# Kernel tuning notes

Hardware: AMD Instinct MI355X
Metric: run time of the kernel (lower is better)

The kernel has to match this reference:

```python
import jax, jax.numpy as jnp
import numpy as np

N_NODES = 50000
N_EDGES = 800000
IN_F, EDGE_F, HID, HEADS, OUT_F = 128, 16, 32, 4, 128
NEG_SLOPE = 0.2


def edge_gat_layer(h, ef, src, dst, W, We, al, ar, ae, b, act):
    """One DGL-style EdgeGATConv layer.
    h: [N, Fin], ef: [E, Fe], W: [Fin, H*D], We: [Fe, H*D],
    al/ar/ae: [H, D], b: [H*D]. Returns [N, H*D].
    """
    N = h.shape[0]
    H, D = al.shape
    feat = (h @ W).reshape(N, H, D)                    # [N,H,D]
    fe = (ef @ We).reshape(-1, H, D)                   # [E,H,D]
    el = jnp.einsum('nhd,hd->nh', feat, al)            # [N,H]
    er = jnp.einsum('nhd,hd->nh', feat, ar)            # [N,H]
    ee = jnp.einsum('ehd,hd->eh', fe, ae)              # [E,H]
    e = jax.nn.leaky_relu(el[src] + er[dst] + ee, NEG_SLOPE)  # [E,H]
    # edge softmax over incoming edges of each dst node
    emax = jax.ops.segment_max(e, dst, num_segments=N)        # [N,H]
    ex = jnp.exp(e - emax[dst])                               # [E,H]
    esum = jax.ops.segment_sum(ex, dst, num_segments=N)       # [N,H]
    a = ex / esum[dst]                                        # [E,H]
    msg = feat[src] * a[:, :, None]                           # [E,H,D]
    rst = jax.ops.segment_sum(msg, dst, num_segments=N)       # [N,H,D]
    rst = rst + b.reshape(1, H, D)
    if act:
        rst = jax.nn.relu(rst)
    return rst.reshape(N, H * D)


def _glorot(k, shape):
    fan = shape[0]
    return jax.random.normal(k, shape, dtype=jnp.float32) / np.sqrt(fan)


def setup_inputs() -> dict:
    key = jax.random.key(0)
    ks = jax.random.split(key, 24)
    inp = {
        'h': jax.random.normal(ks[0], (N_NODES, IN_F), dtype=jnp.float32),
        'edge_feats': jax.random.normal(ks[1], (N_EDGES, EDGE_F), dtype=jnp.float32),
        'src': jax.random.randint(ks[2], (N_EDGES,), 0, N_NODES, dtype=jnp.int32),
        'dst': jax.random.randint(ks[3], (N_EDGES,), 0, N_NODES, dtype=jnp.int32),
    }
    # layer 0: IN_F -> HEADS*HID ; layer 1: HEADS*HID -> HEADS*HID ; layer 2: heads=1, OUT_F
    dims = [(IN_F, HEADS, HID), (HEADS * HID, HEADS, HID), (HEADS * HID, 1, OUT_F)]
    ki = 4
    for i, (fin, H, D) in enumerate(dims):
        inp[f'W{i}'] = _glorot(ks[ki], (fin, H * D)); ki += 1
        inp[f'We{i}'] = _glorot(ks[ki], (EDGE_F, H * D)); ki += 1
        inp[f'al{i}'] = _glorot(ks[ki], (H, D)); ki += 1
        inp[f'ar{i}'] = _glorot(ks[ki], (H, D)); ki += 1
        inp[f'ae{i}'] = _glorot(ks[ki], (H, D)); ki += 1
        inp[f'b{i}'] = jnp.zeros((H * D,), dtype=jnp.float32)
    return inp


def reference(h, edge_feats, src, dst,
              W0, We0, al0, ar0, ae0, b0,
              W1, We1, al1, ar1, ae1, b1,
              W2, We2, al2, ar2, ae2, b2):
    h = edge_gat_layer(h, edge_feats, src, dst, W0, We0, al0, ar0, ae0, b0, True)
    h = edge_gat_layer(h, edge_feats, src, dst, W1, We1, al1, ar1, ae1, b1, True)
    h = edge_gat_layer(h, edge_feats, src, dst, W2, We2, al2, ar2, ae2, b2, False)
    return h
```

## Files before the change

kernel.cpp:

```cpp
#include <hip/hip_runtime.h>
#include <hip/hip_fp16.h>
#include <cstdint>

#define NN 50000
#define NE 800000
static constexpr int HD = 128;
static constexpr int EF_DIM = 16;
static constexpr int SCAN_B = 256;
static constexpr int NPARTS = (NN + SCAN_B - 1) / SCAN_B;

typedef _Float16 f16x4 __attribute__((ext_vector_type(4)));
typedef float f32x4 __attribute__((ext_vector_type(4)));

__global__ __launch_bounds__(256) void k_prep(const float* __restrict__ h,
        const float* __restrict__ We0, const float* __restrict__ ae0,
        const float* __restrict__ We1, const float* __restrict__ ae1,
        const float* __restrict__ We2, const float* __restrict__ ae2,
        const float* __restrict__ W0, const float* __restrict__ W1,
        const float* __restrict__ W2,
        int* __restrict__ deg, float* __restrict__ M,
        _Float16* __restrict__ Wht, _Float16* __restrict__ Xh) {
    const int b = blockIdx.x, t = threadIdx.x;
    if (b < 196) {
        int i = b * 256 + t;
        if (i < NN) deg[i] = 0;
        return;
    }
    if (b < 199) {
        int l = b - 196;
        const float* We = (l == 0) ? We0 : (l == 1) ? We1 : We2;
        const float* ae = (l == 0) ? ae0 : (l == 1) ? ae1 : ae2;
        int H = (l == 2) ? 1 : 4, D = (l == 2) ? 128 : 32;
        if (t < EF_DIM * H) {
            int f = t / H, hh = t % H;
            float s = 0.f;
            for (int d = 0; d < D; d++) s += We[f * HD + hh * D + d] * ae[hh * D + d];
            M[l * 64 + f * H + hh] = s;
        }
        return;
    }
    if (b < 391) {
        int i = (b - 199) * 256 + t;
        int l = i >> 14, rem = i & 16383;
        int n = rem >> 7, k = rem & 127;
        const float* W = (l == 0) ? W0 : (l == 1) ? W1 : W2;
        Wht[(size_t)l * 16384 + n * 128 + k] = (_Float16)W[k * 128 + n];
        return;
    }
    {
        int i = (b - 391) * 256 + t;
        if (i < NN * 32) {
            float4 v = ((const float4*)h)[i];
            f16x4 o = {(_Float16)v.x, (_Float16)v.y, (_Float16)v.z, (_Float16)v.w};
            ((f16x4*)Xh)[i] = o;
        }
    }
}


__global__ void k_hist(const int* __restrict__ dst, int* __restrict__ deg) {
    int e = blockIdx.x * blockDim.x + threadIdx.x;
    if (e < NE) atomicAdd(&deg[dst[e]], 1);
}

__global__ __launch_bounds__(SCAN_B) void k_part(const int* __restrict__ deg,
                                                 int* __restrict__ part) {
    __shared__ int s[SCAN_B];
    int t = threadIdx.x;
    int i = blockIdx.x * SCAN_B + t;
    s[t] = (i < NN) ? deg[i] : 0;
    __syncthreads();
    for (int off = SCAN_B / 2; off > 0; off >>= 1) {
        if (t < off) s[t] += s[t + off];
        __syncthreads();
    }
    if (t == 0) part[blockIdx.x] = s[0];
}

__global__ __launch_bounds__(SCAN_B) void k_scanpart(int* __restrict__ part) {
    __shared__ int s[SCAN_B];
    int t = threadIdx.x;
    int v = (t < NPARTS) ? part[t] : 0;
    s[t] = v;
    __syncthreads();
    for (int off = 1; off < SCAN_B; off <<= 1) {
        int u = (t >= off) ? s[t - off] : 0;
        __syncthreads();
        s[t] += u;
        __syncthreads();
    }
    if (t < NPARTS) part[t] = s[t] - v;
}

__global__ __launch_bounds__(SCAN_B) void k_rowptr(const int* __restrict__ deg,
                                                   const int* __restrict__ part,
                                                   int* __restrict__ row_ptr,
                                                   int* __restrict__ cursor) {
    __shared__ int s[SCAN_B];
    int t = threadIdx.x;
    int i = blockIdx.x * SCAN_B + t;
    int v = (i < NN) ? deg[i] : 0;
    s[t] = v;
    __syncthreads();
    for (int off = 1; off < SCAN_B; off <<= 1) {
        int u = (t >= off) ? s[t - off] : 0;
        __syncthreads();
        s[t] += u;
        __syncthreads();
    }
    int excl = s[t] - v + part[blockIdx.x];
    if (i < NN) { row_ptr[i] = excl; cursor[i] = excl; }
    if (i == NN) row_ptr[NN] = NE;
}

__global__ void k_scatter(const int* __restrict__ src, const int* __restrict__ dst,
                          int* __restrict__ cursor, int2* __restrict__ epr) {
    int e = blockIdx.x * blockDim.x + threadIdx.x;
    if (e >= NE) return;
    int d = dst[e];
    int pos = atomicAdd(&cursor[d], 1);
    epr[pos] = make_int2(e, src[e]);
}

__global__ __launch_bounds__(256) void k_segsort(const int* __restrict__ row_ptr,
                                                 int2* __restrict__ epr) {
    __shared__ int2 seg[4][128];
    const int wave = threadIdx.x >> 6;
    const int lane = threadIdx.x & 63;
    const int n = blockIdx.x * 4 + wave;
    const int start = row_ptr[n];
    const int len = row_ptr[n + 1] - start;
    const bool small = (len > 0 && len <= 128);
    if (small)
        for (int s = lane; s < len; s += 64) seg[wave][s] = epr[start + s];
    __syncthreads();
    if (small) {
        for (int s = lane; s < len; s += 64) {
            int2 me = seg[wave][s];
            int rank = 0;
            for (int j = 0; j < len; j++) {
                int2 o = seg[wave][j];
                rank += (o.y < me.y) || (o.y == me.y && o.x < me.x);
            }
            epr[start + rank] = me;
        }
    }
}

__global__ __launch_bounds__(256) void k_eproj(const float* __restrict__ EFt,
                                               const int2* __restrict__ epr,
                                               const float* __restrict__ M,
                                               _Float16* __restrict__ ep0,
                                               _Float16* __restrict__ ep1,
                                               _Float16* __restrict__ ep2) {
    __shared__ float sM[192];
    int t = threadIdx.x;
    if (t < 192) sM[t] = M[t];
    __syncthreads();
    int i = blockIdx.x * 256 + t;
    if (i >= NE) return;
    int e = epr[i].x;
    float ef[EF_DIM];
    const float4* efp = (const float4*)(EFt + (size_t)e * EF_DIM);
#pragma unroll
    for (int q = 0; q < 4; q++) {
        float4 v = efp[q];
        ef[4 * q] = v.x; ef[4 * q + 1] = v.y; ef[4 * q + 2] = v.z; ef[4 * q + 3] = v.w;
    }
    float o0[4] = {0.f, 0.f, 0.f, 0.f};
    float o1[4] = {0.f, 0.f, 0.f, 0.f};
    float o2 = 0.f;
#pragma unroll
    for (int f = 0; f < EF_DIM; f++) {
        float v = ef[f];
#pragma unroll
        for (int hh = 0; hh < 4; hh++) {
            o0[hh] += v * sM[f * 4 + hh];
            o1[hh] += v * sM[64 + f * 4 + hh];
        }
        o2 += v * sM[128 + f];
    }
    f16x4 a = {(_Float16)o0[0], (_Float16)o0[1], (_Float16)o0[2], (_Float16)o0[3]};
    f16x4 c = {(_Float16)o1[0], (_Float16)o1[1], (_Float16)o1[2], (_Float16)o1[3]};
    ((f16x4*)ep0)[i] = a;
    ((f16x4*)ep1)[i] = c;
    ep2[i] = (_Float16)o2;
}


template <int H>
__global__ __launch_bounds__(256) void k_feat(const _Float16* __restrict__ Xh,
                                              const _Float16* __restrict__ Wht,
                                              const float* __restrict__ al,
                                              const float* __restrict__ ar,
                                              _Float16* __restrict__ Fh,
                                              float* __restrict__ el,
                                              float* __restrict__ er) {
    const int t = threadIdx.x;
    const int lane = t & 63;
    const int wv = t >> 6;
    const int l15 = lane & 15;
    const int kg = lane >> 4;
    const int nbase = blockIdx.x * 64;
    const int arow = nbase + wv * 16 + l15;
    const int rclamp = (arow < NN) ? arow : NN - 1;
    const int ksub = kg * 4;
    f16x4 a[8];
#pragma unroll
    for (int kb = 0; kb < 8; kb++)
        a[kb] = *(const f16x4*)(Xh + (size_t)rclamp * 128 + kb * 16 + ksub);

    const int r0 = nbase + wv * 16 + kg * 4;
    float slp[4][H], srp[4][H];
#pragma unroll
    for (int r = 0; r < 4; r++)
#pragma unroll
        for (int hh = 0; hh < H; hh++) { slp[r][hh] = 0.f; srp[r][hh] = 0.f; }

#pragma unroll
    for (int nt = 0; nt < 8; nt++) {
        f32x4 acc = {0.f, 0.f, 0.f, 0.f};
        const int nc = nt * 16 + l15;
        const _Float16* wp = Wht + (size_t)nc * 128;
#pragma unroll
        for (int kb = 0; kb < 8; kb++) {
            f16x4 bf = *(const f16x4*)(wp + kb * 16 + ksub);
            acc = __builtin_amdgcn_mfma_f32_16x16x16f16(a[kb], bf, acc, 0, 0, 0);
        }
        const float alv = al[nc], arv = ar[nc];
        constexpr int HSEL = 0;
        const int hsel = (H == 4) ? (nt >> 1) : HSEL;
#pragma unroll
        for (int r = 0; r < 4; r++) {
            int ro = r0 + r;
            if (ro < NN) Fh[(size_t)ro * 128 + nc] = (_Float16)acc[r];
            slp[r][hsel] += acc[r] * alv;
            srp[r][hsel] += acc[r] * arv;
        }
    }

#pragma unroll
    for (int m = 1; m < 16; m <<= 1)
#pragma unroll
        for (int r = 0; r < 4; r++)
#pragma unroll
            for (int hh = 0; hh < H; hh++) {
                slp[r][hh] += __shfl_xor(slp[r][hh], m);
                srp[r][hh] += __shfl_xor(srp[r][hh], m);
            }

    if (H == 4) {
        int r = l15 >> 2, hh2 = l15 & 3;
        float sv = 0.f, ev = 0.f;
#pragma unroll
        for (int rr = 0; rr < 4; rr++)
#pragma unroll
            for (int hc = 0; hc < H; hc++)
                if (rr == r && hc == hh2) { sv = slp[rr][hc]; ev = srp[rr][hc]; }
        int ro = r0 + r;
        if (ro < NN) { el[ro * 4 + hh2] = sv; er[ro * 4 + hh2] = ev; }
    } else {
        if (l15 < 4) {
            float sv = 0.f, ev = 0.f;
#pragma unroll
            for (int rr = 0; rr < 4; rr++)
                if (rr == l15) { sv = slp[rr][0]; ev = srp[rr][0]; }
            int ro = r0 + l15;
            if (ro < NN) { el[ro] = sv; er[ro] = ev; }
        }
    }
}

template <int H, int D, int OUT16>
__global__ __launch_bounds__(256) void k_node(const int* __restrict__ row_ptr,
                                              const int2* __restrict__ epr,
                                              const _Float16* __restrict__ ep,
                                              const float* __restrict__ el,
                                              const float* __restrict__ er,
                                              const __half2* __restrict__ Fh,
                                              const float* __restrict__ bias,
                                              float* __restrict__ Rf,
                                              _Float16* __restrict__ Rh,
                                              int act) {
    __shared__ float wlds[4][256];
    const int wave = threadIdx.x >> 6;
    const int lane = threadIdx.x & 63;
    const int n = blockIdx.x * 4 + wave;
    const int start = row_ptr[n];
    const int end = row_ptr[n + 1];
    const int len = end - start;
    const int slots = len * H;
    const int c = 2 * lane;
    const int hcol = c / D;
    float2 b2 = make_float2(bias[c], bias[c + 1]);
    float2 a = make_float2(0.f, 0.f);

    if (len > 0) {
        constexpr int hsh = (H == 4) ? 2 : 0;
        const int hh = lane & (H - 1);
        const float er_j = er[n * H + hh];
        const _Float16* epb = ep + (size_t)start * H;
        float pmax = -3.0e38f, psum = 0.f;

        if (slots <= 256) {
            float* wp = wlds[wave];
            for (int jj = lane; jj < slots; jj += 64) {
                int i = start + (jj >> hsh);
                float x = el[epr[i].y * H + hh] + er_j + (float)epb[jj];
                x = (x > 0.f) ? x : 0.2f * x;
                wp[jj] = x;
                pmax = fmaxf(pmax, x);
            }
            for (int m = H; m < 64; m <<= 1) pmax = fmaxf(pmax, __shfl_xor(pmax, m));
            for (int jj = lane; jj < slots; jj += 64) {
                float ex = __expf(wp[jj] - pmax);
                wp[jj] = ex;
                psum += ex;
            }
            for (int m = H; m < 64; m <<= 1) psum += __shfl_xor(psum, m);
            const float inv = 1.f / __shfl(psum, hcol);
#pragma unroll 4
            for (int i = start; i < end; i++) {
                float w = wp[(i - start) * H + hcol];
                float2 f2 = __half22float2(Fh[(size_t)epr[i].y * 64 + lane]);
                a.x += f2.x * w;
                a.y += f2.y * w;
            }
            a.x *= inv;
            a.y *= inv;
        } else {
            for (int jj = lane; jj < slots; jj += 64) {
                int i = start + (jj >> hsh);
                float x = el[epr[i].y * H + hh] + er_j + (float)epb[jj];
                x = (x > 0.f) ? x : 0.2f * x;
                pmax = fmaxf(pmax, x);
            }
            for (int m = H; m < 64; m <<= 1) pmax = fmaxf(pmax, __shfl_xor(pmax, m));
            for (int jj = lane; jj < slots; jj += 64) {
                int i = start + (jj >> hsh);
                float x = el[epr[i].y * H + hh] + er_j + (float)epb[jj];
                x = (x > 0.f) ? x : 0.2f * x;
                psum += __expf(x - pmax);
            }
            for (int m = H; m < 64; m <<= 1) psum += __shfl_xor(psum, m);
            const float inv = 1.f / __shfl(psum, hcol);
            const float pm_c = __shfl(pmax, hcol);
            const float er_c = er[n * H + hcol];
            for (int i = start; i < end; i++) {
                int sn = epr[i].y;
                float x = el[sn * H + hcol] + er_c + (float)epb[(i - start) * H + hcol];
                x = (x > 0.f) ? x : 0.2f * x;
                float w = __expf(x - pm_c);
                float2 f2 = __half22float2(Fh[(size_t)sn * 64 + lane]);
                a.x += f2.x * w;
                a.y += f2.y * w;
            }
            a.x *= inv;
            a.y *= inv;
        }
    }

    float2 v = make_float2(a.x + b2.x, a.y + b2.y);
    if (act) { v.x = fmaxf(v.x, 0.f); v.y = fmaxf(v.y, 0.f); }
    if (OUT16)
        ((__half2*)Rh)[(size_t)n * 64 + lane] = __floats2half2_rn(v.x, v.y);
    else
        ((float2*)Rf)[(size_t)n * 64 + lane] = v;
}


extern "C" void kernel_launch(void* const* d_in, const int* in_sizes, int n_in,
                              void* d_out, int out_size, void* d_ws, size_t ws_size,
                              hipStream_t stream) {
    const float* h   = (const float*)d_in[0];
    const float* eft = (const float*)d_in[1];
    const int* src   = (const int*)d_in[2];
    const int* dst   = (const int*)d_in[3];
    auto P = [&](int i) { return (const float*)d_in[i]; };

    float* ws = (float*)d_ws;
    _Float16* Fh   = (_Float16*)ws;
    _Float16* Xh   = Fh + (size_t)NN * 128;
    _Float16* Wht  = Xh + (size_t)NN * 128;
    _Float16* ep0  = Wht + 3 * 16384;
    _Float16* ep1  = ep0 + (size_t)NE * 4;
    _Float16* ep2  = ep1 + (size_t)NE * 4;
    float* el      = (float*)(ep2 + NE);
    float* er      = el + (size_t)NN * 4;
    float* M       = er + (size_t)NN * 4;
    int2* epr      = (int2*)(M + 192);
    int* row_ptr   = (int*)(epr + NE);
    int* cursor    = row_ptr + (NN + 1);
    int* deg       = cursor + NN;
    int* part      = deg + NN;
    float* out     = (float*)d_out;

    hipLaunchKernelGGL(k_prep, dim3(391 + (NN * 32 + 255) / 256), dim3(256), 0, stream,
                       h, P(5), P(8), P(11), P(14), P(17), P(20),
                       P(4), P(10), P(16), deg, M, Wht, Xh);
    hipLaunchKernelGGL(k_hist, dim3((NE + 255) / 256), dim3(256), 0, stream, dst, deg);
    hipLaunchKernelGGL(k_part, dim3(NPARTS), dim3(SCAN_B), 0, stream, deg, part);
    hipLaunchKernelGGL(k_scanpart, dim3(1), dim3(SCAN_B), 0, stream, part);
    hipLaunchKernelGGL(k_rowptr, dim3(NPARTS), dim3(SCAN_B), 0, stream,
                       deg, part, row_ptr, cursor);
    hipLaunchKernelGGL(k_scatter, dim3((NE + 255) / 256), dim3(256), 0, stream,
                       src, dst, cursor, epr);
    hipLaunchKernelGGL(k_segsort, dim3(NN / 4), dim3(256), 0, stream, row_ptr, epr);
    hipLaunchKernelGGL(k_eproj, dim3((NE + 255) / 256), dim3(256), 0, stream,
                       eft, epr, M, ep0, ep1, ep2);

    const int FG = (NN + 63) / 64;
    hipLaunchKernelGGL((k_feat<4>), dim3(FG), dim3(256), 0, stream,
                       Xh, Wht, P(6), P(7), Fh, el, er);
    hipLaunchKernelGGL((k_node<4, 32, 1>), dim3(NN / 4), dim3(256), 0, stream,
                       row_ptr, epr, ep0, el, er, (const __half2*)Fh, P(9),
                       nullptr, Xh, 1);
    hipLaunchKernelGGL((k_feat<4>), dim3(FG), dim3(256), 0, stream,
                       Xh, Wht + 16384, P(12), P(13), Fh, el, er);
    hipLaunchKernelGGL((k_node<4, 32, 1>), dim3(NN / 4), dim3(256), 0, stream,
                       row_ptr, epr, ep1, el, er, (const __half2*)Fh, P(15),
                       nullptr, Xh, 1);
    hipLaunchKernelGGL((k_feat<1>), dim3(FG), dim3(256), 0, stream,
                       Xh, Wht + 32768, P(18), P(19), Fh, el, er);
    hipLaunchKernelGGL((k_node<1, 128, 0>), dim3(NN / 4), dim3(256), 0, stream,
                       row_ptr, epr, ep2, el, er, (const __half2*)Fh, P(21),
                       out, nullptr, 0);
}
```

Measured before the change: 411.1 us.

## Fuse edge projection into CSR scatter and emit sorted SoA edge arrays

The edge-feature projection now runs inside the scatter kernel, in original edge order. Each edge's src, id and fp16 projections for all three layers are written as a padded 64-byte record at its CSR slot. The segment-sort kernel then ranks these records and writes sorted SoA arrays (ssrc, ep0/ep1/ep2). The separate k_eproj launch and its gathered edge-feature reads go away, and the node kernels read a 4-byte src index instead of an int2. The cost is heavier scattered writes: 64 bytes per edge, half of them zero padding. The record buffer also reuses workspace shared with Fh/el/er.

```diff
diff --git a/kernel.cpp b/kernel.cpp
--- a/kernel.cpp
+++ b/kernel.cpp
@@ -11,6 +11,16 @@
 
 typedef _Float16 f16x4 __attribute__((ext_vector_type(4)));
 typedef float f32x4 __attribute__((ext_vector_type(4)));
+
+struct RecP {
+    int src;
+    int e;
+    f16x4 p0;
+    f16x4 p1;
+    _Float16 p2;
+    _Float16 pad;
+};
+union Rec32 { RecP r; float4 v[2]; };
 
 __global__ __launch_bounds__(256) void k_prep(const float* __restrict__ h,
         const float* __restrict__ We0, const float* __restrict__ ae0,
@@ -113,18 +123,61 @@
     if (i == NN) row_ptr[NN] = NE;
 }
 
-__global__ void k_scatter(const int* __restrict__ src, const int* __restrict__ dst,
-                          int* __restrict__ cursor, int2* __restrict__ epr) {
-    int e = blockIdx.x * blockDim.x + threadIdx.x;
+__global__ __launch_bounds__(256) void k_scat64(const int* __restrict__ src,
+                                                const int* __restrict__ dst,
+                                                const float* __restrict__ EFt,
+                                                const float* __restrict__ M,
+                                                int* __restrict__ cursor,
+                                                float4* __restrict__ rec) {
+    __shared__ float sM[192];
+    int t = threadIdx.x;
+    if (t < 192) sM[t] = M[t];
+    __syncthreads();
+    int e = blockIdx.x * 256 + t;
     if (e >= NE) return;
+    float ef[EF_DIM];
+    const float4* efp = (const float4*)(EFt + (size_t)e * EF_DIM);
+#pragma unroll
+    for (int q = 0; q < 4; q++) {
+        float4 v = efp[q];
+        ef[4 * q] = v.x; ef[4 * q + 1] = v.y; ef[4 * q + 2] = v.z; ef[4 * q + 3] = v.w;
+    }
+    float o0[4] = {0.f, 0.f, 0.f, 0.f};
+    float o1[4] = {0.f, 0.f, 0.f, 0.f};
+    float o2 = 0.f;
+#pragma unroll
+    for (int f = 0; f < EF_DIM; f++) {
+        float v = ef[f];
+#pragma unroll
+        for (int hh = 0; hh < 4; hh++) {
+            o0[hh] += v * sM[f * 4 + hh];
+            o1[hh] += v * sM[64 + f * 4 + hh];
+        }
+        o2 += v * sM[128 + f];
+    }
+    Rec32 u;
+    u.r.src = src[e];
+    u.r.e = e;
+    u.r.p0 = f16x4{(_Float16)o0[0], (_Float16)o0[1], (_Float16)o0[2], (_Float16)o0[3]};
+    u.r.p1 = f16x4{(_Float16)o1[0], (_Float16)o1[1], (_Float16)o1[2], (_Float16)o1[3]};
+    u.r.p2 = (_Float16)o2;
+    u.r.pad = (_Float16)0.f;
     int d = dst[e];
     int pos = atomicAdd(&cursor[d], 1);
-    epr[pos] = make_int2(e, src[e]);
-}
-
-__global__ __launch_bounds__(256) void k_segsort(const int* __restrict__ row_ptr,
-                                                 int2* __restrict__ epr) {
-    __shared__ int2 seg[4][128];
+    float4* p = rec + (size_t)pos * 4;
+    p[0] = u.v[0];
+    p[1] = u.v[1];
+    p[2] = make_float4(0.f, 0.f, 0.f, 0.f);
+    p[3] = make_float4(0.f, 0.f, 0.f, 0.f);
+}
+
+__global__ __launch_bounds__(256) void k_segsort2(const int* __restrict__ row_ptr,
+                                                  const float4* __restrict__ rec,
+                                                  int* __restrict__ ssrc,
+                                                  f16x4* __restrict__ ep0,
+                                                  f16x4* __restrict__ ep1,
+                                                  _Float16* __restrict__ ep2) {
+    __shared__ Rec32 seg[4][128];
     const int wave = threadIdx.x >> 6;
     const int lane = threadIdx.x & 63;
     const int n = blockIdx.x * 4 + wave;
@@ -132,59 +185,37 @@
     const int len = row_ptr[n + 1] - start;
     const bool small = (len > 0 && len <= 128);
     if (small)
-        for (int s = lane; s < len; s += 64) seg[wave][s] = epr[start + s];
+        for (int s = lane; s < len; s += 64) {
+            seg[wave][s].v[0] = rec[(size_t)(start + s) * 4];
+            seg[wave][s].v[1] = rec[(size_t)(start + s) * 4 + 1];
+        }
     __syncthreads();
     if (small) {
         for (int s = lane; s < len; s += 64) {
-            int2 me = seg[wave][s];
+            RecP me = seg[wave][s].r;
             int rank = 0;
             for (int j = 0; j < len; j++) {
-                int2 o = seg[wave][j];
-                rank += (o.y < me.y) || (o.y == me.y && o.x < me.x);
-            }
-            epr[start + rank] = me;
-        }
-    }
-}
-
-__global__ __launch_bounds__(256) void k_eproj(const float* __restrict__ EFt,
-                                               const int2* __restrict__ epr,
-                                               const float* __restrict__ M,
-                                               _Float16* __restrict__ ep0,
-                                               _Float16* __restrict__ ep1,
-                                               _Float16* __restrict__ ep2) {
-    __shared__ float sM[192];
-    int t = threadIdx.x;
-    if (t < 192) sM[t] = M[t];
-    __syncthreads();
-    int i = blockIdx.x * 256 + t;
-    if (i >= NE) return;
-    int e = epr[i].x;
-    float ef[EF_DIM];
-    const float4* efp = (const float4*)(EFt + (size_t)e * EF_DIM);
-#pragma unroll
-    for (int q = 0; q < 4; q++) {
-        float4 v = efp[q];
-        ef[4 * q] = v.x; ef[4 * q + 1] = v.y; ef[4 * q + 2] = v.z; ef[4 * q + 3] = v.w;
-    }
-    float o0[4] = {0.f, 0.f, 0.f, 0.f};
-    float o1[4] = {0.f, 0.f, 0.f, 0.f};
-    float o2 = 0.f;
-#pragma unroll
-    for (int f = 0; f < EF_DIM; f++) {
-        float v = ef[f];
-#pragma unroll
-        for (int hh = 0; hh < 4; hh++) {
-            o0[hh] += v * sM[f * 4 + hh];
-            o1[hh] += v * sM[64 + f * 4 + hh];
-        }
-        o2 += v * sM[128 + f];
-    }
-    f16x4 a = {(_Float16)o0[0], (_Float16)o0[1], (_Float16)o0[2], (_Float16)o0[3]};
-    f16x4 c = {(_Float16)o1[0], (_Float16)o1[1], (_Float16)o1[2], (_Float16)o1[3]};
-    ((f16x4*)ep0)[i] = a;
-    ((f16x4*)ep1)[i] = c;
-    ep2[i] = (_Float16)o2;
+                const RecP& o = seg[wave][j].r;
+                rank += (o.src < me.src) || (o.src == me.src && o.e < me.e);
+            }
+            int w = start + rank;
+            ssrc[w] = me.src;
+            ep0[w] = me.p0;
+            ep1[w] = me.p1;
+            ep2[w] = me.p2;
+        }
+    } else if (len > 128) {
+        for (int s = lane; s < len; s += 64) {
+            Rec32 u;
+            u.v[0] = rec[(size_t)(start + s) * 4];
+            u.v[1] = rec[(size_t)(start + s) * 4 + 1];
+            int w = start + s;
+            ssrc[w] = u.r.src;
+            ep0[w] = u.r.p0;
+            ep1[w] = u.r.p1;
+            ep2[w] = u.r.p2;
+        }
+    }
 }
 
 
@@ -273,7 +304,7 @@
 
 template <int H, int D, int OUT16>
 __global__ __launch_bounds__(256) void k_node(const int* __restrict__ row_ptr,
-                                              const int2* __restrict__ epr,
+                                              const int* __restrict__ ssrc,
                                               const _Float16* __restrict__ ep,
                                               const float* __restrict__ el,
                                               const float* __restrict__ er,
@@ -306,7 +337,7 @@
             float* wp = wlds[wave];
             for (int jj = lane; jj < slots; jj += 64) {
                 int i = start + (jj >> hsh);
-                float x = el[epr[i].y * H + hh] + er_j + (float)epb[jj];
+                float x = el[ssrc[i] * H + hh] + er_j + (float)epb[jj];
                 x = (x > 0.f) ? x : 0.2f * x;
                 wp[jj] = x;
                 pmax = fmaxf(pmax, x);
@@ -322,7 +353,7 @@
 #pragma unroll 4
             for (int i = start; i < end; i++) {
                 float w = wp[(i - start) * H + hcol];
-                float2 f2 = __half22float2(Fh[(size_t)epr[i].y * 64 + lane]);
+                float2 f2 = __half22float2(Fh[(size_t)ssrc[i] * 64 + lane]);
                 a.x += f2.x * w;
                 a.y += f2.y * w;
             }
@@ -331,14 +362,14 @@
         } else {
             for (int jj = lane; jj < slots; jj += 64) {
                 int i = start + (jj >> hsh);
-                float x = el[epr[i].y * H + hh] + er_j + (float)epb[jj];
+                float x = el[ssrc[i] * H + hh] + er_j + (float)epb[jj];
                 x = (x > 0.f) ? x : 0.2f * x;
                 pmax = fmaxf(pmax, x);
             }
             for (int m = H; m < 64; m <<= 1) pmax = fmaxf(pmax, __shfl_xor(pmax, m));
             for (int jj = lane; jj < slots; jj += 64) {
                 int i = start + (jj >> hsh);
-                float x = el[epr[i].y * H + hh] + er_j + (float)epb[jj];
+                float x = el[ssrc[i] * H + hh] + er_j + (float)epb[jj];
                 x = (x > 0.f) ? x : 0.2f * x;
                 psum += __expf(x - pmax);
             }
@@ -347,7 +378,7 @@
             const float pm_c = __shfl(pmax, hcol);
             const float er_c = er[n * H + hcol];
             for (int i = start; i < end; i++) {
-                int sn = epr[i].y;
+                int sn = ssrc[i];
                 float x = el[sn * H + hcol] + er_c + (float)epb[(i - start) * H + hcol];
                 x = (x > 0.f) ? x : 0.2f * x;
                 float w = __expf(x - pm_c);
@@ -379,17 +410,18 @@
     auto P = [&](int i) { return (const float*)d_in[i]; };
 
     float* ws = (float*)d_ws;
+    float4* rec    = (float4*)ws;
     _Float16* Fh   = (_Float16*)ws;
-    _Float16* Xh   = Fh + (size_t)NN * 128;
-    _Float16* Wht  = Xh + (size_t)NN * 128;
-    _Float16* ep0  = Wht + 3 * 16384;
-    _Float16* ep1  = ep0 + (size_t)NE * 4;
-    _Float16* ep2  = ep1 + (size_t)NE * 4;
-    float* el      = (float*)(ep2 + NE);
-    float* er      = el + (size_t)NN * 4;
-    float* M       = er + (size_t)NN * 4;
-    int2* epr      = (int2*)(M + 192);
-    int* row_ptr   = (int*)(epr + NE);
+    float* el      = ws + 3200000;
+    float* er      = ws + 3400000;
+    _Float16* Xh   = (_Float16*)(ws + 12800000);
+    _Float16* Wht  = (_Float16*)(ws + 16000000);
+    _Float16* ep0s = Wht + 3 * 16384;
+    _Float16* ep1s = ep0s + (size_t)NE * 4;
+    _Float16* ep2s = ep1s + (size_t)NE * 4;
+    int* ssrc      = (int*)(ep2s + NE);
+    float* M       = (float*)(ssrc + NE);
+    int* row_ptr   = (int*)(M + 192);
     int* cursor    = row_ptr + (NN + 1);
     int* deg       = cursor + NN;
     int* part      = deg + NN;
@@ -403,26 +435,25 @@
     hipLaunchKernelGGL(k_scanpart, dim3(1), dim3(SCAN_B), 0, stream, part);
     hipLaunchKernelGGL(k_rowptr, dim3(NPARTS), dim3(SCAN_B), 0, stream,
                        deg, part, row_ptr, cursor);
-    hipLaunchKernelGGL(k_scatter, dim3((NE + 255) / 256), dim3(256), 0, stream,
-                       src, dst, cursor, epr);
-    hipLaunchKernelGGL(k_segsort, dim3(NN / 4), dim3(256), 0, stream, row_ptr, epr);
-    hipLaunchKernelGGL(k_eproj, dim3((NE + 255) / 256), dim3(256), 0, stream,
-                       eft, epr, M, ep0, ep1, ep2);
+    hipLaunchKernelGGL(k_scat64, dim3((NE + 255) / 256), dim3(256), 0, stream,
+                       src, dst, eft, M, cursor, rec);
+    hipLaunchKernelGGL(k_segsort2, dim3(NN / 4), dim3(256), 0, stream,
+                       row_ptr, rec, ssrc, (f16x4*)ep0s, (f16x4*)ep1s, ep2s);
 
     const int FG = (NN + 63) / 64;
     hipLaunchKernelGGL((k_feat<4>), dim3(FG), dim3(256), 0, stream,
                        Xh, Wht, P(6), P(7), Fh, el, er);
     hipLaunchKernelGGL((k_node<4, 32, 1>), dim3(NN / 4), dim3(256), 0, stream,
-                       row_ptr, epr, ep0, el, er, (const __half2*)Fh, P(9),
+                       row_ptr, ssrc, ep0s, el, er, (const __half2*)Fh, P(9),
                        nullptr, Xh, 1);
     hipLaunchKernelGGL((k_feat<4>), dim3(FG), dim3(256), 0, stream,
                        Xh, Wht + 16384, P(12), P(13), Fh, el, er);
     hipLaunchKernelGGL((k_node<4, 32, 1>), dim3(NN / 4), dim3(256), 0, stream,
-                       row_ptr, epr, ep1, el, er, (const __half2*)Fh, P(15),
+                       row_ptr, ssrc, ep1s, el, er, (const __half2*)Fh, P(15),
                        nullptr, Xh, 1);
     hipLaunchKernelGGL((k_feat<1>), dim3(FG), dim3(256), 0, stream,
                        Xh, Wht + 32768, P(18), P(19), Fh, el, er);
     hipLaunchKernelGGL((k_node<1, 128, 0>), dim3(NN / 4), dim3(256), 0, stream,
-                       row_ptr, epr, ep2, el, er, (const __half2*)Fh, P(21),
+                       row_ptr, ssrc, ep2s, el, er, (const __half2*)Fh, P(21),
                        out, nullptr, 0);
 }
```

After: 391.2 us. 4.8% less time.
